# Optimization experiments

Hardware: AMD Instinct MI355X
Metric: run time of the kernel (lower is better)

Reference implementation:

```python
import jax, jax.numpy as jnp
import numpy as np
from jax import lax

H = 12  # num_heads (from init_kwargs)


def _orthogonal_landmarks(q, num_landmarks):
    # q: (B, N, D) already scaled. Faithful to torch loop: recursively pick the
    # point whose max |cos sim| to the already-selected landmarks is minimal.
    B, N, D = q.shape
    nrm = jnp.linalg.norm(q, axis=-1, keepdims=True)
    qk = q / jnp.maximum(nrm, 1e-12)
    bidx = jnp.arange(B)
    key = jax.random.key(42)
    idx0 = jax.random.randint(key, (B,), 0, N)
    cur = qk[bidx, idx0]                             # (B, D)
    # running max |cos sim|; selected rows pinned to 10 (as in torch code)
    max_sim = jnp.zeros((B, N), qk.dtype).at[bidx, idx0].set(10.0)

    def step(carry, _):
        max_sim, cur = carry
        cos = jnp.abs(jnp.einsum('bnd,bd->bn', qk, cur))
        max_sim = jnp.maximum(max_sim, cos)
        idx = jnp.argmin(max_sim, axis=-1)
        cur2 = qk[bidx, idx]
        max_sim = max_sim.at[bidx, idx].set(10.0)
        return (max_sim, cur2), idx

    (_, _), idxs = lax.scan(step, (max_sim, cur), None, length=num_landmarks - 1)
    all_idx = jnp.concatenate([idx0[None, :], idxs], axis=0).T  # (B, L)
    landmarks = q[bidx[:, None], all_idx]                        # unnormalized q rows
    return lax.stop_gradient(landmarks)


def _orthoformer(q, k, v, num_landmarks, num_frames):
    # q,k,v: (B*h, N, D);  N = F * P
    Bh, N, D = q.shape
    F = num_frames
    P = N // F
    sc = D ** (-0.25)
    q = q * sc
    k = k * sc
    lm = _orthogonal_landmarks(q, num_landmarks)                 # (Bh, L, D)
    kernel_1 = jax.nn.softmax(jnp.einsum('bnd,bld->bnl', q, lm), axis=-1)   # (Bh,N,L)
    k2 = jnp.einsum('bld,bnd->bln', lm, k).reshape(Bh, num_landmarks, F, P)
    kernel_2 = jax.nn.softmax(k2, axis=-1)                       # (Bh,L,F,P)
    vr = v.reshape(Bh, F, P, D)
    x = jnp.einsum('blfp,bfpd->blfd', kernel_2, vr)
    x = jnp.einsum('bnl,blfd->bnfd', kernel_1, x)                # (Bh,N,F,D)
    return x


def setup_inputs() -> dict:
    key = jax.random.key(0)
    ks = jax.random.split(key, 6)
    B, F, P, C = 2, 16, 196, 768
    N = F * P
    s = 0.02
    x = jax.random.normal(ks[0], (B, N, C), jnp.float32)
    W_qkv = jax.random.normal(ks[1], (C, 3 * C), jnp.float32) * s
    W_pq = jax.random.normal(ks[2], (C, C), jnp.float32) * s
    W_pkv = jax.random.normal(ks[3], (C, 2 * C), jnp.float32) * s
    W_proj = jax.random.normal(ks[4], (C, C), jnp.float32) * s
    b_proj = jnp.zeros((C,), jnp.float32)
    return {"x": x, "W_qkv": W_qkv, "W_pq": W_pq, "W_pkv": W_pkv,
            "W_proj": W_proj, "b_proj": b_proj,
            "seq_len": P, "num_frames": F, "num_landmarks": 128}


def reference(x, W_qkv, W_pq, W_pkv, W_proj, b_proj, seq_len, num_frames, num_landmarks):
    B, N, C = x.shape
    F, P, h = num_frames, seq_len, H
    d = C // h
    scale = d ** (-0.5)
    qkv = x @ W_qkv                                              # (B,N,3C)
    q, k, v = jnp.split(qkv, 3, axis=-1)
    def to_bh(t):  # b n (h d) -> (b h) n d
        return t.reshape(B, N, h, d).transpose(0, 2, 1, 3).reshape(B * h, N, d)
    q_, k_, v_ = to_bh(q), to_bh(k), to_bh(v)
    xo = _orthoformer(q_, k_, v_, num_landmarks, F)              # (B*h,N,F,d)
    # (b h) s f d -> b s f (h d)
    xo = xo.reshape(B, h, N, F, d).transpose(0, 2, 3, 1, 4).reshape(B, N, F, C)
    # diagonal over (frame-of-query g, frame-of-key f)
    xd = xo.reshape(B, F, P, F, C)
    xdiag = jnp.diagonal(xd, axis1=1, axis2=3)                   # (B,P,C,F)
    xdiag = jnp.moveaxis(xdiag, -1, 1).reshape(B, N, C)          # b (f p) d
    q2 = xdiag @ W_pq                                            # (B,N,C)
    k2, v2 = jnp.split(xo @ W_pkv, 2, axis=-1)                   # (B,N,F,C) each
    q2 = q2.reshape(B, N, h, d).transpose(0, 2, 1, 3) * scale    # (B,h,N,d)
    k2 = k2.reshape(B, N, F, h, d).transpose(0, 3, 1, 2, 4)      # (B,h,N,F,d)
    v2 = v2.reshape(B, N, F, h, d).transpose(0, 3, 1, 2, 4)
    attn = jax.nn.softmax(jnp.einsum('bhsd,bhsfd->bhsf', q2, k2), axis=-1)
    out = jnp.einsum('bhsf,bhsfd->bhsd', attn, v2)               # (B,h,N,d)
    out = out.transpose(0, 2, 1, 3).reshape(B, N, C)
    out = out @ W_proj + b_proj
    return out, attn
```

## Files before the change

kernel.cpp:

```cpp
#include <hip/hip_runtime.h>


using u16 = unsigned short;
using u32 = unsigned int;
using u64 = unsigned long long;

typedef short bf16x8 __attribute__((ext_vector_type(8)));
typedef float f32x4 __attribute__((ext_vector_type(4)));

#define N_ 3136
#define C_ 768
#define H_ 12
#define F_ 16
#define P_ 196
#define L_ 128
#define SC_ 0.35355339059327373f
#define OUTPART_ ((size_t)2 * N_ * C_)
#define KB_ 8
#define RPB_ 392

__device__ __forceinline__ float b2f(u16 u) {
  u32 x = ((u32)u) << 16; float f; __builtin_memcpy(&f, &x, 4); return f;
}
__device__ __forceinline__ float lo16f(u32 u) {
  u32 x = u << 16; float f; __builtin_memcpy(&f, &x, 4); return f;
}
__device__ __forceinline__ float hi16f(u32 u) {
  u32 x = u & 0xFFFF0000u; float f; __builtin_memcpy(&f, &x, 4); return f;
}
__device__ __forceinline__ u16 f2b(float f) {
  u32 u; __builtin_memcpy(&u, &f, 4);
  u32 r = (u + 0x7FFFu + ((u >> 16) & 1u)) >> 16;
  return (u16)r;
}
__device__ __forceinline__ u64 d2u(double d) { u64 u; __builtin_memcpy(&u, &d, 8); return u; }

__device__ __forceinline__ void gll16(const void* g, void* l) {
  __builtin_amdgcn_global_load_lds(
      (__attribute__((address_space(1))) void*)g,
      (__attribute__((address_space(3))) void*)l, 16, 0, 0);
}

__global__ void detect_k(const u32* __restrict__ w, int* __restrict__ flag) {
  const int t = threadIdx.x;
  int hits = 0;
  #pragma unroll
  for (int i = 0; i < 16; ++i) {
    u32 word = w[t * 16 + i];
    u32 e = (word >> 7) & 0xFFu;
    if (e >= 110u && e <= 126u) hits++;
  }
  #pragma unroll
  for (int off = 32; off > 0; off >>= 1) hits += __shfl_down(hits, off);
  if (t == 0) flag[0] = (hits >= 512) ? 0 : 1;
}

__global__ void zcnt_k(u64* __restrict__ p) { if (threadIdx.x < 384) p[threadIdx.x] = 0ull; }

__device__ __forceinline__ void tf2(u32 k0, u32 k1v, u32 c0, u32 c1, u32& o0, u32& o1) {
  u32 ks[3] = {k0, k1v, k0 ^ k1v ^ 0x1BD11BDAu};
  u32 x0 = c0 + ks[0], x1 = c1 + ks[1];
  const u32 rA[4] = {13u, 15u, 26u, 6u}, rB[4] = {17u, 29u, 16u, 24u};
  #pragma unroll
  for (int r = 0; r < 5; ++r) {
    #pragma unroll
    for (int q = 0; q < 4; ++q) {
      u32 rot = (r & 1) ? rB[q] : rA[q];
      x0 += x1; x1 = (x1 << rot) | (x1 >> (32u - rot)); x1 ^= x0;
    }
    x0 += ks[(r + 1) % 3];
    x1 += ks[(r + 2) % 3] + (u32)(r + 1);
  }
  o0 = x0; o1 = x1;
}

__device__ __forceinline__ int tf_idx0(int bh) {
  u32 a0, a1, b0, b1;
  tf2(0u, 42u, 0u, 0u, a0, a1);
  tf2(0u, 42u, 0u, 1u, b0, b1);
  u32 j = (u32)bh;
  u32 h0, h1, l0, l1;
  tf2(a0, a1, 0u, j, h0, h1);
  u32 hi = h0 ^ h1;
  tf2(b0, b1, 0u, j, l0, l1);
  u32 lo = l0 ^ l1;
  return (int)(((hi % 3136u) * 2048u + (lo % 3136u)) % 3136u);
}

__device__ __forceinline__ void qsel_body(const void* xr, const void* wr, int f32i,
                                          float* qt, int m0, int n0, int t,
                                          float* As, float* Bs)
{
  const int tx = t & 15, ty = t >> 4;
  float acc[8][4];
  #pragma unroll
  for (int i = 0; i < 8; ++i)
    #pragma unroll
    for (int j = 0; j < 4; ++j) acc[i][j] = 0.f;

  const int alr = t >> 1;
  const int alk = (t & 1) * 8;
  const int bkr = t >> 4;
  const int bnc = (t & 15) * 4;

  for (int k0 = 0; k0 < 768; k0 += 16) {
    float av[8];
    float4 bv;
    if (f32i) {
      const float* xa = (const float*)xr + (size_t)(m0 + alr) * 768 + k0 + alk;
      float4 a0 = *(const float4*)(xa);
      float4 a1 = *(const float4*)(xa + 4);
      av[0] = a0.x; av[1] = a0.y; av[2] = a0.z; av[3] = a0.w;
      av[4] = a1.x; av[5] = a1.y; av[6] = a1.z; av[7] = a1.w;
      bv = *(const float4*)((const float*)wr + (size_t)(k0 + bkr) * 2304 + n0 + bnc);
    } else {
      const u16* xa = (const u16*)xr + (size_t)(m0 + alr) * 768 + k0 + alk;
      #pragma unroll
      for (int j = 0; j < 8; ++j) av[j] = b2f(xa[j]);
      const u16* wa = (const u16*)wr + (size_t)(k0 + bkr) * 2304 + n0 + bnc;
      bv.x = b2f(wa[0]); bv.y = b2f(wa[1]); bv.z = b2f(wa[2]); bv.w = b2f(wa[3]);
    }
    #pragma unroll
    for (int j = 0; j < 8; ++j) As[alr * 20 + alk + j] = av[j];
    *(float4*)(&Bs[bkr * 64 + bnc]) = bv;
    __syncthreads();
    #pragma unroll
    for (int kk = 0; kk < 16; ++kk) {
      float a[8], b[4];
      #pragma unroll
      for (int i = 0; i < 8; ++i) a[i] = As[(ty * 8 + i) * 20 + kk];
      #pragma unroll
      for (int j = 0; j < 4; ++j) b[j] = Bs[kk * 64 + tx * 4 + j];
      #pragma unroll
      for (int i = 0; i < 8; ++i)
        #pragma unroll
        for (int j = 0; j < 4; ++j) acc[i][j] += a[i] * b[j];
    }
    __syncthreads();
  }
  #pragma unroll
  for (int i = 0; i < 8; ++i) {
    const int m = m0 + ty * 8 + i;
    const int b = m / N_, n = m - b * N_;
    #pragma unroll
    for (int j = 0; j < 4; ++j) {
      const int col = n0 + tx * 4 + j;
      const int hh = col >> 6, dd = col & 63;
      qt[((size_t)(b * H_ + hh) * 64 + dd) * N_ + n] = acc[i][j] * SC_;
    }
  }
}

__global__ __launch_bounds__(256) void qselT_k(const void* __restrict__ xr, const void* __restrict__ wr,
                                               const int* __restrict__ flagp, float* __restrict__ qt)
{
  __shared__ float As[128 * 20];
  __shared__ float Bs[16 * 64];
  qsel_body(xr, wr, flagp[0], qt, blockIdx.x * 128, blockIdx.y * 64, threadIdx.x, As, Bs);
}

__device__ __forceinline__ void twT_body(const void* W, int K, int Nn, int f32i,
                                         u16* WT, int k0, int n0, int t, u16 (&Ts)[64][80])
{
  const int kr = t >> 2, nc = (t & 3) * 16;
  u16 tmp[16];
  if (f32i) {
    const float* p = (const float*)W + (size_t)(k0 + kr) * Nn + n0 + nc;
    #pragma unroll
    for (int j = 0; j < 16; ++j) tmp[j] = f2b(p[j]);
  } else {
    const u16* p = (const u16*)W + (size_t)(k0 + kr) * Nn + n0 + nc;
    #pragma unroll
    for (int j = 0; j < 16; ++j) tmp[j] = p[j];
  }
  #pragma unroll
  for (int j = 0; j < 16; ++j) Ts[kr][nc + j] = tmp[j];
  __syncthreads();
  const int nr = t >> 2, kc = (t & 3) * 16;
  u16 o[16];
  #pragma unroll
  for (int j = 0; j < 16; ++j) o[j] = Ts[kc + j][nr];
  u16* dst = WT + (size_t)(n0 + nr) * K + k0 + kc;
  *(uint4*)(dst) = *(uint4*)(o);
  *(uint4*)(dst + 8) = *(uint4*)(o + 8);
}

__global__ __launch_bounds__(256) void twT_k(const void* __restrict__ W, int K, int Nn,
                                             const int* __restrict__ flagp, u16* __restrict__ WT)
{
  __shared__ u16 Ts[64][80];
  twT_body(W, K, Nn, flagp[0], WT, blockIdx.x * 64, blockIdx.y * 64, threadIdx.x, Ts);
}

__global__ __launch_bounds__(256) void twT3_k(const void* __restrict__ W0, const void* __restrict__ W1,
                                              const void* __restrict__ W2, const int* __restrict__ flagp,
                                              u16* __restrict__ T0, u16* __restrict__ T1, u16* __restrict__ T2,
                                              u16* __restrict__ Wb)
{
  __shared__ u16 Ts[64][80];
  const int z = blockIdx.z;
  const int t = threadIdx.x;
  if (z == 3) {
    const int k0 = blockIdx.x * 64, n0 = blockIdx.y * 64;
    const int kr = t >> 2, nc = (t & 3) * 16;
    u16 tmp[16];
    if (flagp[0]) {
      const float* p = (const float*)W0 + (size_t)(k0 + kr) * 1536 + n0 + nc;
      #pragma unroll
      for (int j = 0; j < 16; ++j) tmp[j] = f2b(p[j]);
    } else {
      const u16* p = (const u16*)W0 + (size_t)(k0 + kr) * 1536 + n0 + nc;
      #pragma unroll
      for (int j = 0; j < 16; ++j) tmp[j] = p[j];
    }
    u16* dst = Wb + (size_t)(k0 + kr) * 1536 + n0 + nc;
    *(uint4*)(dst) = *(uint4*)(tmp);
    *(uint4*)(dst + 8) = *(uint4*)(tmp + 8);
    return;
  }
  const void* W = (z == 0) ? W0 : (z == 1) ? W1 : W2;
  u16* WT = (z == 0) ? T0 : (z == 1) ? T1 : T2;
  const int Nn = (z == 0) ? 1536 : 768;
  if (blockIdx.y * 64 >= Nn) return;
  twT_body(W, 768, Nn, flagp[0], WT, blockIdx.x * 64, blockIdx.y * 64, t, Ts);
}

__device__ __forceinline__ void xcvt_body(const void* x, int f32i, u16* xb, int i)
{
  if (f32i) {
    const float4* p = (const float4*)x + (size_t)i * 2;
    float4 f0 = p[0], f1 = p[1];
    u16 tmp[8] = { f2b(f0.x), f2b(f0.y), f2b(f0.z), f2b(f0.w),
                   f2b(f1.x), f2b(f1.y), f2b(f1.z), f2b(f1.w) };
    *(uint4*)(xb + (size_t)i * 8) = *(uint4*)tmp;
  } else {
    ((uint4*)xb)[i] = ((const uint4*)x)[i];
  }
}

__global__ __launch_bounds__(256) void xcvt_k(const void* __restrict__ x,
                                              const int* __restrict__ flagp, u16* __restrict__ xb)
{
  xcvt_body(x, flagp[0], xb, blockIdx.x * 256 + threadIdx.x);
}

__global__ __launch_bounds__(256) void fusedA_k(const void* __restrict__ x, const void* __restrict__ Wqkv,
                                                const int* __restrict__ flagp, float* __restrict__ qt,
                                                u16* __restrict__ WqkvT, u16* __restrict__ xb)
{
  __shared__ float As[128 * 20];
  __shared__ float Bs[16 * 64];
  __shared__ u16 Ts[64][80];
  const int id = blockIdx.x;
  const int t = threadIdx.x;
  const int f32i = flagp[0];
  if (id < 588) {
    qsel_body(x, Wqkv, f32i, qt, (id % 49) * 128, (id / 49) * 64, t, As, Bs);
  } else if (id < 1020) {
    const int id2 = id - 588;
    twT_body(Wqkv, 768, 2304, f32i, WqkvT, (id2 % 12) * 64, (id2 / 12) * 64, t, Ts);
  } else {
    xcvt_body(x, f32i, xb, (id - 1020) * 256 + t);
  }
}

struct GemmCore {
  const u16 *aP0, *aP1, *bP0, *bP1;
  u16 *lA0, *lA1, *lB0, *lB1;
  int roA[4], roB[4];
  int mw, nw, lr, lk;
};

__device__ __forceinline__ void gemm_core_init(GemmCore& gc, u16* As, u16* Bs,
    const u16* A16, const u16* B16, size_t aOff, size_t bOff,
    int m0, int n0, int lda, int ldb, int M, int t)
{
  const int lane = t & 63;
  const int w = t >> 6;
  gc.mw = (w >> 1) * 64;
  gc.nw = (w & 1) * 64;
  gc.lr = lane & 15;
  gc.lk = lane >> 4;
  const int c0 = w * 2, c1 = c0 + 1;
  const int rl = lane >> 2, sl = lane & 3;
  const int rowA0 = c0 * 16 + rl, rowA1 = c1 * 16 + rl;
  const int segA0 = (sl ^ ((rowA0 ^ (rowA0 >> 2)) & 3)) * 8;
  const int segA1 = (sl ^ ((rowA1 ^ (rowA1 >> 2)) & 3)) * 8;
  int ga0 = m0 + rowA0; if (ga0 >= M) ga0 = M - 1;
  int ga1 = m0 + rowA1; if (ga1 >= M) ga1 = M - 1;
  gc.aP0 = A16 + aOff + (size_t)ga0 * lda + segA0;
  gc.aP1 = A16 + aOff + (size_t)ga1 * lda + segA1;
  gc.bP0 = B16 + bOff + (size_t)(n0 + rowA0) * ldb + segA0;
  gc.bP1 = B16 + bOff + (size_t)(n0 + rowA1) * ldb + segA1;
  gc.lA0 = &As[c0 * 512]; gc.lA1 = &As[c1 * 512];
  gc.lB0 = &Bs[c0 * 512]; gc.lB1 = &Bs[c1 * 512];
  #pragma unroll
  for (int q = 0; q < 4; ++q) {
    const int ra = gc.mw + q * 16 + gc.lr;
    gc.roA[q] = ra * 32 + ((gc.lk ^ ((ra ^ (ra >> 2)) & 3)) * 8);
    const int rb = gc.nw + q * 16 + gc.lr;
    gc.roB[q] = rb * 32 + ((gc.lk ^ ((rb ^ (rb >> 2)) & 3)) * 8);
  }
}

__device__ __forceinline__ void gemm_core_loop(const GemmCore& gc, u16* As, u16* Bs,
                                               int K, f32x4 (&acc)[4][4])
{
  for (int k0 = 0; k0 < K; k0 += 32) {
    gll16(gc.aP0 + k0, gc.lA0);
    gll16(gc.aP1 + k0, gc.lA1);
    gll16(gc.bP0 + k0, gc.lB0);
    gll16(gc.bP1 + k0, gc.lB1);
    __syncthreads();
    bf16x8 af[4], bfv[4];
    #pragma unroll
    for (int mt = 0; mt < 4; ++mt) af[mt] = *(const bf16x8*)(&As[gc.roA[mt]]);
    #pragma unroll
    for (int nt = 0; nt < 4; ++nt) bfv[nt] = *(const bf16x8*)(&Bs[gc.roB[nt]]);
    #pragma unroll
    for (int mt = 0; mt < 4; ++mt)
      #pragma unroll
      for (int nt = 0; nt < 4; ++nt)
        acc[mt][nt] = __builtin_amdgcn_mfma_f32_16x16x32_bf16(af[mt], bfv[nt], acc[mt][nt], 0, 0, 0);
    __syncthreads();
  }
}

__device__ __forceinline__ void mode0_epi(const f32x4 (&acc)[4][4], int m0, int n0,
                                          int mw, int nw, int lr, int lk,
                                          u16* ob0, u16* ob1, u16* ob2)
{
  #pragma unroll
  for (int mt = 0; mt < 4; ++mt) {
    #pragma unroll
    for (int nt = 0; nt < 4; ++nt) {
      #pragma unroll
      for (int r = 0; r < 4; ++r) {
        const int grow = m0 + mw + mt * 16 + lk * 4 + r;
        const int gcol = n0 + nw + nt * 16 + lr;
        float vv = acc[mt][nt][r];
        int b = (grow >= N_) ? 1 : 0;
        int n = grow - b * N_;
        int t3 = gcol / C_, cc = gcol - t3 * C_;
        int hh = cc >> 6, dd = cc & 63;
        size_t dst = (((size_t)(b * H_ + hh)) * N_ + n) * 64 + dd;
        if (t3 == 0) ob0[dst] = f2b(vv * SC_);
        else if (t3 == 1) ob1[dst] = f2b(vv * SC_);
        else ob2[dst] = f2b(vv);
      }
    }
  }
}

__global__ __launch_bounds__(512, 1) void fusedB_k(
    const float* __restrict__ qt, float* __restrict__ lm, u64* __restrict__ cand,
    const u16* __restrict__ xb, const u16* __restrict__ WqkvT,
    u16* __restrict__ qb, u16* __restrict__ kbuf, u16* __restrict__ vb)
{
  __shared__ double curD[64];
  __shared__ u64 redV[8];
  __shared__ int redI[8];
  __shared__ int sW;
  __shared__ u16 As[128 * 32];
  __shared__ u16 Bs[128 * 32];
  const int t = threadIdx.x;

  if (blockIdx.x >= 192) {
    const int gid = blockIdx.x - 192;
    const int m0 = (gid % 49) * 128;
    const int n0 = (gid / 49) * 128;
    if (t < 256) {
      f32x4 acc[4][4];
      #pragma unroll
      for (int i = 0; i < 4; ++i)
        #pragma unroll
        for (int j = 0; j < 4; ++j) acc[i][j] = (f32x4){0.f, 0.f, 0.f, 0.f};
      GemmCore gc;
      gemm_core_init(gc, As, Bs, xb, WqkvT, 0, 0, m0, n0, 768, 768, 6272, t);
      gemm_core_loop(gc, As, Bs, 768, acc);
      mode0_epi(acc, m0, n0, gc.mw, gc.nw, gc.lr, gc.lk, qb, kbuf, vb);
    } else {
      for (int i = 0; i < 24; ++i) { __syncthreads(); __syncthreads(); }
    }
    return;
  }

  const int bh = blockIdx.x % 24;
  const int kb = blockIdx.x / 24;
  const float* QT = qt + (size_t)bh * 64 * N_;
  float* LM = lm + (size_t)bh * L_ * 64;
  u64* cd = cand + (size_t)bh * 16;
  const bool act = (t < RPB_);
  const int g = t >> 2, dc = t & 3, d0 = dc * 16;
  const int r0 = kb * RPB_;
  const int myRow = r0 + t;
  const float* base = QT + r0 + 4 * g;

  float4 qreg[16];
  #pragma unroll
  for (int i = 0; i < 16; ++i) qreg[i] = (float4){0.f, 0.f, 0.f, 0.f};
  if (act) {
    #pragma unroll
    for (int i = 0; i < 16; ++i) qreg[i] = *(const float4*)(base + (size_t)(d0 + i) * N_);
  }

  double inv_own = 0.0, ms_own = 0.0;
  if (act) {
    double s0 = 0.0, s1 = 0.0, s2 = 0.0, s3 = 0.0;
    #pragma unroll
    for (int i = 0; i < 16; ++i) {
      const float4 v = qreg[i];
      s0 += (double)v.x * (double)v.x; s1 += (double)v.y * (double)v.y;
      s2 += (double)v.z * (double)v.z; s3 += (double)v.w * (double)v.w;
    }
    s0 += __shfl_xor(s0, 1); s1 += __shfl_xor(s1, 1);
    s2 += __shfl_xor(s2, 1); s3 += __shfl_xor(s3, 1);
    s0 += __shfl_xor(s0, 2); s1 += __shfl_xor(s1, 2);
    s2 += __shfl_xor(s2, 2); s3 += __shfl_xor(s3, 2);
    const double sown = (dc == 0) ? s0 : (dc == 1) ? s1 : (dc == 2) ? s2 : s3;
    inv_own = 1.0 / fmax(sqrt(sown), 1e-12);
  }
  const int idx0 = tf_idx0(bh);
  if (act && myRow == idx0) ms_own = 10.0;

  if (t < 64) {
    const float vf = QT[(size_t)t * N_ + idx0];
    double v = (double)vf;
    double s = v * v;
    #pragma unroll
    for (int off = 32; off; off >>= 1) s += __shfl_xor(s, off);
    curD[t] = v / fmax(sqrt(s), 1e-12);
    if (kb == 0) LM[t] = vf;
  }
  __syncthreads();

  for (int step = 1; step < 128; ++step) {
    u64 bV = d2u(1e30); int bI = 0x7fffffff;
    if (act) {
      double a0 = 0.0, a1 = 0.0, a2 = 0.0, a3 = 0.0;
      #pragma unroll
      for (int i = 0; i < 16; ++i) {
        const float4 v = qreg[i];
        const double c = curD[d0 + i];
        a0 += (double)v.x * c; a1 += (double)v.y * c;
        a2 += (double)v.z * c; a3 += (double)v.w * c;
      }
      a0 += __shfl_xor(a0, 1); a1 += __shfl_xor(a1, 1);
      a2 += __shfl_xor(a2, 1); a3 += __shfl_xor(a3, 1);
      a0 += __shfl_xor(a0, 2); a1 += __shfl_xor(a1, 2);
      a2 += __shfl_xor(a2, 2); a3 += __shfl_xor(a3, 2);
      const double aown = (dc == 0) ? a0 : (dc == 1) ? a1 : (dc == 2) ? a2 : a3;
      ms_own = fmax(ms_own, fabs(aown * inv_own));
      bV = d2u(ms_own); bI = myRow;
    }
    #pragma unroll
    for (int off = 32; off; off >>= 1) {
      const u64 ov = __shfl_xor(bV, off);
      const int oi = __shfl_xor(bI, off);
      if (ov < bV || (ov == bV && oi < bI)) { bV = ov; bI = oi; }
    }
    if ((t & 63) == 0) { redV[t >> 6] = bV; redI[t >> 6] = bI; }
    __syncthreads();
    const int par = step & 1;
    if (t == 0) {
      u64 v = redV[0]; int ix = redI[0];
      #pragma unroll
      for (int w2 = 1; w2 < 8; ++w2)
        if (redV[w2] < v || (redV[w2] == v && redI[w2] < ix)) { v = redV[w2]; ix = redI[w2]; }
      const u64 pk = (v & ~((1ull << 19) - 1ull)) | ((u64)(u32)(step & 127) << 12) | (u64)(u32)ix;
      __hip_atomic_store(&cd[par * KB_ + kb], pk, __ATOMIC_RELAXED, __HIP_MEMORY_SCOPE_AGENT);
    }
    if (t < 64) {
      u64 pv = ~0ull;
      int ok = 1;
      for (;;) {
        if (t < KB_) {
          pv = __hip_atomic_load(&cd[par * KB_ + t], __ATOMIC_RELAXED, __HIP_MEMORY_SCOPE_AGENT);
          ok = ((int)((pv >> 12) & 127u) == step) ? 1 : 0;
        }
        if (__all(ok)) break;
        __builtin_amdgcn_s_sleep(1);
      }
      u64 m = (t < KB_) ? pv : ~0ull;
      #pragma unroll
      for (int off = 1; off < KB_; off <<= 1) {
        const u64 o = __shfl_xor(m, off);
        if (o < m) m = o;
      }
      if (t == 0) sW = (int)(m & 0xFFFu);
    }
    __syncthreads();
    const int w = sW;
    if (act && myRow == w) ms_own = 10.0;
    if (t < 64) {
      const float vf = QT[(size_t)t * N_ + w];
      double v = (double)vf;
      double s = v * v;
      #pragma unroll
      for (int off = 32; off; off >>= 1) s += __shfl_xor(s, off);
      curD[t] = v / fmax(sqrt(s), 1e-12);
      if (kb == 0) LM[(size_t)step * 64 + t] = vf;
    }
    __syncthreads();
  }
}

template <int MODE>
__global__ __launch_bounds__(256) void gemm_k(
    const void* __restrict__ Ap, const void* __restrict__ Bp,
    int M, int K, int lda, int ldb, int n0c, int cn, const int* __restrict__ flagp,
    float* __restrict__ of0, u16* __restrict__ ob0, u16* __restrict__ ob1, u16* __restrict__ ob2,
    const void* __restrict__ biasRaw, void* __restrict__ outRaw)
{
  __shared__ u16 As[128 * 32];
  __shared__ u16 Bs[128 * 32];
  const int t = threadIdx.x;
  const int m0 = blockIdx.x * 128;
  const int n0 = blockIdx.y * 128;
  const int rf = (MODE == 4) ? flagp[0] : 0;

  size_t aOff = 0, bOff = 0;
  if constexpr (MODE == 1) {
    const int bh = blockIdx.z;
    aOff = (size_t)bh * ((size_t)N_ * 128) + (size_t)n0c * 128;
    bOff = (size_t)bh * (1024 * 128);
  }
  if constexpr (MODE == 5) {
    const int h = blockIdx.z;
    aOff = (size_t)h * (2 * cn) * 64;
    bOff = (size_t)h * 64;
  }
  if constexpr (MODE == 6) {
    const int h = blockIdx.z;
    aOff = (size_t)h * (2 * cn) * 768;
    bOff = (size_t)(768 + h * 64) * 768;
  }
  f32x4 acc[4][4];
  #pragma unroll
  for (int i = 0; i < 4; ++i)
    #pragma unroll
    for (int j = 0; j < 4; ++j) acc[i][j] = (f32x4){0.f, 0.f, 0.f, 0.f};

  GemmCore gc;
  gemm_core_init(gc, As, Bs, (const u16*)Ap, (const u16*)Bp, aOff, bOff, m0, n0, lda, ldb, M, t);
  gemm_core_loop(gc, As, Bs, K, acc);

  const int lr = gc.lr, lk = gc.lk, mw = gc.mw, nw = gc.nw;
  if constexpr (MODE == 0) {
    mode0_epi(acc, m0, n0, mw, nw, lr, lk, ob0, ob1, ob2);
    return;
  }
  #pragma unroll
  for (int mt = 0; mt < 4; ++mt) {
    #pragma unroll
    for (int nt = 0; nt < 4; ++nt) {
      #pragma unroll
      for (int r = 0; r < 4; ++r) {
        const int grow = m0 + mw + mt * 16 + lk * 4 + r;
        const int gcol = n0 + nw + nt * 16 + lr;
        if (grow >= M) continue;
        float vv = acc[mt][nt][r];
        if constexpr (MODE == 1) {
          const int bh = blockIdx.z;
          int b = bh / H_, hh = bh - b * H_;
          int f = gcol >> 6, dd = gcol & 63;
          u16 wv = f2b(vv);
          ob0[(((size_t)(b * cn + grow)) * F_ + f) * C_ + hh * 64 + dd] = wv;
          int n = n0c + grow;
          if (f == n / P_) ob1[((size_t)(b * cn + grow)) * C_ + hh * 64 + dd] = wv;
        } else if constexpr (MODE == 3) {
          int hh = gcol >> 6, dd = gcol & 63;
          ob0[((size_t)hh * (2 * cn) + grow) * 64 + dd] = f2b(vv * 0.125f);
        } else if constexpr (MODE == 5) {
          ob0[((size_t)blockIdx.z * (2 * cn) + grow) * 768 + gcol] = f2b(vv);
        } else if constexpr (MODE == 6) {
          if (gcol < 64) {
            int b2 = (grow >= cn) ? 1 : 0;
            int ln = grow - b2 * cn;
            ob0[((size_t)(b2 * N_ + n0c + ln)) * 768 + blockIdx.z * 64 + gcol] = f2b(vv);
          }
        } else {
          float bvad = rf ? ((const float*)biasRaw)[gcol] : b2f(((const u16*)biasRaw)[gcol]);
          float ov = vv + bvad;
          if (rf) ((float*)outRaw)[(size_t)grow * C_ + gcol] = ov;
          else    ((u16*)outRaw)[(size_t)grow * C_ + gcol] = f2b(ov);
        }
      }
    }
  }
}

__global__ __launch_bounds__(256) void k1_k(const u16* __restrict__ qb,
                                            const float* __restrict__ lm,
                                            u16* __restrict__ k1)
{
  const int bh = blockIdx.y;
  const int r0 = blockIdx.x * 64;
  __shared__ float qT[64][65];
  __shared__ float lmS[128 * 64];
  __shared__ float redA[4][64];
  __shared__ float redB[64];
  const int t = threadIdx.x;
  const u16* Q = qb + ((size_t)bh * N_ + r0) * 64;
  const float* Lm = lm + (size_t)bh * L_ * 64;
  for (int u = t; u < 2048; u += 256) ((float4*)lmS)[u] = ((const float4*)Lm)[u];
  for (int u = t; u < 512; u += 256) {
    int row = u >> 3, j0 = (u & 7) * 8;
    uint4 pk = *(const uint4*)(Q + (size_t)row * 64 + j0);
    const u16* pu = (const u16*)&pk;
    #pragma unroll
    for (int jj = 0; jj < 8; ++jj) qT[j0 + jj][row] = b2f(pu[jj]);
  }
  __syncthreads();
  const int row = t & 63, ch = t >> 6;
  float qr[64];
  #pragma unroll
  for (int j = 0; j < 64; ++j) qr[j] = qT[j][row];
  float s[32];
  for (int li = 0; li < 32; ++li) {
    const float* lp = lmS + (ch * 32 + li) * 64;
    float a = 0.f;
    #pragma unroll
    for (int j = 0; j < 64; ++j) a += lp[j] * qr[j];
    s[li] = a;
  }
  float mx = -1e30f;
  for (int li = 0; li < 32; ++li) mx = fmaxf(mx, s[li]);
  redA[ch][row] = mx;
  __syncthreads();
  if (t < 64) redB[t] = fmaxf(fmaxf(redA[0][t], redA[1][t]), fmaxf(redA[2][t], redA[3][t]));
  __syncthreads();
  mx = redB[row];
  float sum = 0.f;
  for (int li = 0; li < 32; ++li) { float e = __expf(s[li] - mx); s[li] = e; sum += e; }
  __syncthreads();
  redA[ch][row] = sum;
  __syncthreads();
  if (t < 64) redB[t] = 1.0f / (redA[0][t] + redA[1][t] + redA[2][t] + redA[3][t]);
  __syncthreads();
  const float inv = redB[row];
  u16* out = k1 + ((size_t)bh * N_ + r0 + row) * 128 + ch * 32;
  for (int li = 0; li < 32; ++li) out[li] = f2b(s[li] * inv);
}

__global__ __launch_bounds__(256) void k2x1_k(const float* __restrict__ lm,
                                              const u16* __restrict__ kb,
                                              const u16* __restrict__ vb,
                                              u16* __restrict__ x1)
{
  const int bh = blockIdx.x;
  const int f = blockIdx.y;
  __shared__ u16 kS[P_ * 64];
  __shared__ u16 vS[P_ * 64];
  __shared__ float redM[2][128];
  __shared__ float redS[2][128];
  const int t = threadIdx.x;
  const u16* Kf = kb + ((size_t)bh * N_ + f * P_) * 64;
  const u16* Vf = vb + ((size_t)bh * N_ + f * P_) * 64;
  for (int u = t; u < 1568; u += 256) {
    ((uint4*)kS)[u] = ((const uint4*)Kf)[u];
    ((uint4*)vS)[u] = ((const uint4*)Vf)[u];
  }
  __syncthreads();
  const int l = t & 127, half = t >> 7;
  const float* lp = lm + ((size_t)bh * L_ + l) * 64;
  float lr[64];
  #pragma unroll
  for (int j = 0; j < 64; ++j) lr[j] = lp[j];

  const int p0 = half * 98, p1 = p0 + 98;
  float mx = -1e30f;
  for (int p = p0; p < p1; ++p) {
    const uint4* kp = (const uint4*)(kS + p * 64);
    float s = 0.f;
    #pragma unroll
    for (int q4 = 0; q4 < 8; ++q4) {
      uint4 pk = kp[q4];
      const u32* pu = (const u32*)&pk;
      #pragma unroll
      for (int j2 = 0; j2 < 4; ++j2) {
        u32 u = pu[j2];
        s += lr[q4 * 8 + j2 * 2] * lo16f(u) + lr[q4 * 8 + j2 * 2 + 1] * hi16f(u);
      }
    }
    mx = fmaxf(mx, s);
  }
  redM[half][l] = mx;
  __syncthreads();
  mx = fmaxf(redM[0][l], redM[1][l]);

  float sm = 0.f;
  for (int p = p0; p < p1; ++p) {
    const uint4* kp = (const uint4*)(kS + p * 64);
    float s = 0.f;
    #pragma unroll
    for (int q4 = 0; q4 < 8; ++q4) {
      uint4 pk = kp[q4];
      const u32* pu = (const u32*)&pk;
      #pragma unroll
      for (int j2 = 0; j2 < 4; ++j2) {
        u32 u = pu[j2];
        s += lr[q4 * 8 + j2 * 2] * lo16f(u) + lr[q4 * 8 + j2 * 2 + 1] * hi16f(u);
      }
    }
    sm += __expf(s - mx);
  }
  redS[half][l] = sm;
  __syncthreads();
  const float inv = 1.0f / (redS[0][l] + redS[1][l]);

  const int dd0 = half * 32;
  float acc[32];
  #pragma unroll
  for (int u = 0; u < 32; ++u) acc[u] = 0.f;
  for (int p = 0; p < P_; ++p) {
    const uint4* kp = (const uint4*)(kS + p * 64);
    float s = 0.f;
    #pragma unroll
    for (int q4 = 0; q4 < 8; ++q4) {
      uint4 pk = kp[q4];
      const u32* pu = (const u32*)&pk;
      #pragma unroll
      for (int j2 = 0; j2 < 4; ++j2) {
        u32 u = pu[j2];
        s += lr[q4 * 8 + j2 * 2] * lo16f(u) + lr[q4 * 8 + j2 * 2 + 1] * hi16f(u);
      }
    }
    const float e = __expf(s - mx);
    const uint4* vp = (const uint4*)(vS + p * 64 + dd0);
    #pragma unroll
    for (int q4 = 0; q4 < 4; ++q4) {
      uint4 pv = vp[q4];
      const u32* pu = (const u32*)&pv;
      #pragma unroll
      for (int j2 = 0; j2 < 4; ++j2) {
        u32 u = pu[j2];
        acc[q4 * 8 + j2 * 2]     += e * lo16f(u);
        acc[q4 * 8 + j2 * 2 + 1] += e * hi16f(u);
      }
    }
  }
  u16* outT = x1 + (size_t)bh * (1024 * 128) + (size_t)(f * 64 + dd0) * 128 + l;
  for (int u = 0; u < 32; ++u) outT[(size_t)u * 128] = f2b(acc[u] * inv);
}

__global__ __launch_bounds__(256) void attn2_k(const u16* __restrict__ xoc,
                                               const u16* __restrict__ g,
                                               int n0c, int cn, const int* __restrict__ flagp,
                                               void* __restrict__ outRaw, u16* __restrict__ wc)
{
  __shared__ float aS[12][16];
  const int t = threadIdx.x;
  const int m = blockIdx.x;
  const int b = (m >= cn) ? 1 : 0;
  const int ln = m - b * cn;
  const int n = n0c + ln;
  const int f32o = flagp[0];
  const u16* Xo = xoc + ((size_t)(b * cn + ln) * 16) * 768;
  const size_t hstr = (size_t)(2 * cn) * 768;

  if (t < 192) {
    const int h = t >> 4, f = t & 15;
    const uint4* xp = (const uint4*)(Xo + (size_t)f * 768);
    const uint4* gp = (const uint4*)(g + (size_t)h * hstr + (size_t)m * 768);
    float lg = 0.f;
    #pragma unroll 4
    for (int q = 0; q < 96; ++q) {
      uint4 xv = xp[q], gv = gp[q];
      const u32* xu = (const u32*)&xv;
      const u32* gu = (const u32*)&gv;
      #pragma unroll
      for (int j = 0; j < 4; ++j)
        lg += lo16f(xu[j]) * lo16f(gu[j]) + hi16f(xu[j]) * hi16f(gu[j]);
    }
    float mx = lg;
    mx = fmaxf(mx, __shfl_xor(mx, 1));
    mx = fmaxf(mx, __shfl_xor(mx, 2));
    mx = fmaxf(mx, __shfl_xor(mx, 4));
    mx = fmaxf(mx, __shfl_xor(mx, 8));
    float e = __expf(lg - mx);
    float sm = e;
    sm += __shfl_xor(sm, 1);
    sm += __shfl_xor(sm, 2);
    sm += __shfl_xor(sm, 4);
    sm += __shfl_xor(sm, 8);
    const float a = e / sm;
    const size_t abase = ((size_t)(b * H_ + h) * N_ + n) * F_ + f;
    if (f32o) ((float*)outRaw)[OUTPART_ + abase] = a;
    else      ((u16*)outRaw)[OUTPART_ + abase] = f2b(a);
    aS[h][f] = a;
  }
  __syncthreads();
  if (t < 192) {
    const int cg = t >> 1, sh = t & 1;
    const int c0 = cg * 8;
    float acc[6][8];
    #pragma unroll
    for (int j = 0; j < 6; ++j)
      #pragma unroll
      for (int k = 0; k < 8; ++k) acc[j][k] = 0.f;
    for (int f = 0; f < 16; ++f) {
      uint4 xv = *(const uint4*)(Xo + (size_t)f * 768 + c0);
      const u32* xu = (const u32*)&xv;
      float xf[8];
      #pragma unroll
      for (int j = 0; j < 4; ++j) { xf[2 * j] = lo16f(xu[j]); xf[2 * j + 1] = hi16f(xu[j]); }
      #pragma unroll
      for (int j = 0; j < 6; ++j) {
        const float a = aS[sh * 6 + j][f];
        #pragma unroll
        for (int k = 0; k < 8; ++k) acc[j][k] += a * xf[k];
      }
    }
    #pragma unroll
    for (int j = 0; j < 6; ++j) {
      u16 pk[8];
      #pragma unroll
      for (int k = 0; k < 8; ++k) pk[k] = f2b(acc[j][k]);
      *(uint4*)(wc + (size_t)(sh * 6 + j) * hstr + (size_t)m * 768 + c0) = *(uint4*)pk;
    }
  }
}

extern "C" void kernel_launch(void* const* d_in, const int* in_sizes, int n_in,
                              void* d_out, int out_size, void* d_ws, size_t ws_size,
                              hipStream_t stream)
{
  (void)in_sizes; (void)n_in; (void)out_size;
  const void* x     = d_in[0];
  const void* Wqkv  = d_in[1];
  const void* Wpq   = d_in[2];
  const void* Wpkv  = d_in[3];
  const void* Wproj = d_in[4];
  const void* bproj = d_in[5];

  char* ws = (char*)d_ws;
  size_t off = 0;
  auto alloc = [&](size_t bytes) { void* p = ws + off; off += (bytes + 255) & ~(size_t)255; return p; };
  int*  flagp  = (int*)alloc(256);
  u16*  WpkvT  = (u16*)alloc(2359296);
  u16*  WpqT   = (u16*)alloc(1179648);
  u16*  WprojT = (u16*)alloc(1179648);
  u16*  Wpkvb  = (u16*)alloc(2359296);
  float* lm    = (float*)alloc(786432);
  u16*  x1b    = (u16*)alloc(6291456);
  u16*  k1b    = (u16*)alloc(19267584);
  const size_t sc0 = off;

  const size_t r1 = sc0;
  const size_t r2 = r1 + 19267584 + 3072;
  const size_t r3 = r2 + 3538944 + 9633792;
  const size_t bigNeed = r3 + 3 * (size_t)9633792 + 256;
  const bool fused = (bigNeed <= ws_size);

  float* qt;  u64* cand;  u16 *WqkvT, *xb, *qb, *kbuf, *vb, *ob;
  size_t chunkBase;
  if (fused) {
    qt    = (float*)(ws + r1);
    cand  = (u64*)(ws + r1 + 19267584);
    WqkvT = (u16*)(ws + r2);
    xb    = WqkvT + 1769472;
    qb    = (u16*)(ws + r3);
    kbuf  = qb + 4816896;
    vb    = kbuf + 4816896;
    ob    = (u16*)(ws + sc0);
    chunkBase = sc0 + 9633792;
  } else {
    qt    = (float*)(ws + sc0);
    cand  = (u64*)(ws + sc0 + 19267584);
    WqkvT = (u16*)(ws + sc0);
    xb    = (u16*)(ws + sc0 + 3538944);
    qb    = (u16*)(ws + sc0 + 13172736);
    kbuf  = qb + 4816896;
    vb    = kbuf + 4816896;
    ob    = (u16*)(ws + sc0);
    chunkBase = sc0 + 9633792;
    if (sc0 + 42074112 + 1024 > ws_size) return;
  }

  int Nc = 0;
  {
    const int cands[5] = {3136, 1568, 784, 392, 196};
    for (int i = 0; i < 5; ++i) {
      if (chunkBase + (size_t)92160 * cands[i] + 1024 <= ws_size) { Nc = cands[i]; break; }
    }
  }
  if (Nc == 0) return;
  const int nchunks = N_ / Nc;
  u16* xoc = (u16*)(ws + chunkBase);
  u16* xdc = xoc + (size_t)24576 * Nc;
  u16* q2b = xdc + (size_t)1536 * Nc;
  u16* gbf = q2b + (size_t)1536 * Nc;

  detect_k<<<1, 64, 0, stream>>>((const u32*)Wqkv, flagp);
  zcnt_k<<<1, 512, 0, stream>>>(cand);
  twT3_k<<<dim3(12, 24, 4), 256, 0, stream>>>(Wpkv, Wpq, Wproj, flagp,
                                              WpkvT, WpqT, WprojT, Wpkvb);

  if (fused) {
    fusedA_k<<<3372, 256, 0, stream>>>(x, Wqkv, flagp, qt, WqkvT, xb);
    fusedB_k<<<1074, 512, 0, stream>>>(qt, lm, cand, xb, WqkvT, qb, kbuf, vb);
  } else {
    qselT_k<<<dim3(49, 12), 256, 0, stream>>>(x, Wqkv, flagp, qt);
    fusedB_k<<<192, 512, 0, stream>>>(qt, lm, cand, xb, WqkvT, qb, kbuf, vb);
    twT_k<<<dim3(12, 36), 256, 0, stream>>>(Wqkv, 768, 2304, flagp, WqkvT);
    xcvt_k<<<2352, 256, 0, stream>>>(x, flagp, xb);
    gemm_k<0><<<dim3(49, 18, 1), 256, 0, stream>>>(xb, WqkvT, 6272, 768, 768, 768, 0, 0, flagp,
                                                   nullptr, qb, kbuf, vb, nullptr, nullptr);
  }

  k2x1_k<<<dim3(24, 16), 256, 0, stream>>>(lm, kbuf, vb, x1b);
  k1_k<<<dim3(49, 24), 256, 0, stream>>>(qb, lm, k1b);

  const int gx = (2 * Nc + 127) / 128;
  for (int c = 0; c < nchunks; ++c) {
    const int n0c = c * Nc;
    gemm_k<1><<<dim3((Nc + 127) / 128, 8, 24), 256, 0, stream>>>(
        k1b, x1b, Nc, 128, 128, 128, n0c, Nc, flagp, nullptr, xoc, xdc, nullptr, nullptr, nullptr);
    gemm_k<3><<<dim3(gx, 6, 1), 256, 0, stream>>>(
        xdc, WpqT, 2 * Nc, 768, 768, 768, n0c, Nc, flagp, nullptr, q2b, nullptr, nullptr, nullptr, nullptr);
    gemm_k<5><<<dim3(gx, 6, 12), 256, 0, stream>>>(
        q2b, Wpkvb, 2 * Nc, 64, 64, 1536, n0c, Nc, flagp, nullptr, gbf, nullptr, nullptr, nullptr, nullptr);
    attn2_k<<<dim3(2 * Nc), 256, 0, stream>>>(xoc, gbf, n0c, Nc, flagp, d_out, gbf);
    gemm_k<6><<<dim3(gx, 1, 12), 256, 0, stream>>>(
        gbf, WpkvT, 2 * Nc, 768, 768, 768, n0c, Nc, flagp, nullptr, ob, nullptr, nullptr, nullptr, nullptr);
  }
  gemm_k<4><<<dim3(49, 6, 1), 256, 0, stream>>>(ob, WprojT, 6272, 768, 768, 768, 0, 0, flagp,
                                                nullptr, nullptr, nullptr, nullptr, bproj, d_out);
}
```

Before: 1.483 ms.

## Fuse weight prep into fusedA, merge k1/k2x1 kernels, relocate ob buffer

Folds the three projection-weight transposes and the Wpkv bf16 copy into the fusedA launch, and merges the k2x1 and k1 kernels into a single fusedC launch with shared memory carved from one buffer. This cuts launch count and lets independent small kernels share the GPU instead of running back-to-back with idle tails. It also moves the ob buffer to the end of the workspace and changes the chunk-size candidates, so the chunked post-attention loop now runs at most 1568 rows per chunk, always at least two chunks. The fused kernels use a larger static shared-memory footprint for every block, which may lower occupancy for the lighter branches.

```diff
diff --git a/kernel.cpp b/kernel.cpp
--- a/kernel.cpp
+++ b/kernel.cpp
@@ -192,6 +192,25 @@
   twT_body(W, K, Nn, flagp[0], WT, blockIdx.x * 64, blockIdx.y * 64, threadIdx.x, Ts);
 }
 
+__device__ __forceinline__ void wpkvb_body(const void* W0, int f32i, u16* Wb,
+                                           int k0, int n0, int t)
+{
+  const int kr = t >> 2, nc = (t & 3) * 16;
+  u16 tmp[16];
+  if (f32i) {
+    const float* p = (const float*)W0 + (size_t)(k0 + kr) * 1536 + n0 + nc;
+    #pragma unroll
+    for (int j = 0; j < 16; ++j) tmp[j] = f2b(p[j]);
+  } else {
+    const u16* p = (const u16*)W0 + (size_t)(k0 + kr) * 1536 + n0 + nc;
+    #pragma unroll
+    for (int j = 0; j < 16; ++j) tmp[j] = p[j];
+  }
+  u16* dst = Wb + (size_t)(k0 + kr) * 1536 + n0 + nc;
+  *(uint4*)(dst) = *(uint4*)(tmp);
+  *(uint4*)(dst + 8) = *(uint4*)(tmp + 8);
+}
+
 __global__ __launch_bounds__(256) void twT3_k(const void* __restrict__ W0, const void* __restrict__ W1,
                                               const void* __restrict__ W2, const int* __restrict__ flagp,
                                               u16* __restrict__ T0, u16* __restrict__ T1, u16* __restrict__ T2,
@@ -201,21 +220,7 @@
   const int z = blockIdx.z;
   const int t = threadIdx.x;
   if (z == 3) {
-    const int k0 = blockIdx.x * 64, n0 = blockIdx.y * 64;
-    const int kr = t >> 2, nc = (t & 3) * 16;
-    u16 tmp[16];
-    if (flagp[0]) {
-      const float* p = (const float*)W0 + (size_t)(k0 + kr) * 1536 + n0 + nc;
-      #pragma unroll
-      for (int j = 0; j < 16; ++j) tmp[j] = f2b(p[j]);
-    } else {
-      const u16* p = (const u16*)W0 + (size_t)(k0 + kr) * 1536 + n0 + nc;
-      #pragma unroll
-      for (int j = 0; j < 16; ++j) tmp[j] = p[j];
-    }
-    u16* dst = Wb + (size_t)(k0 + kr) * 1536 + n0 + nc;
-    *(uint4*)(dst) = *(uint4*)(tmp);
-    *(uint4*)(dst + 8) = *(uint4*)(tmp + 8);
+    wpkvb_body(W0, flagp[0], Wb, blockIdx.x * 64, blockIdx.y * 64, t);
     return;
   }
   const void* W = (z == 0) ? W0 : (z == 1) ? W1 : W2;
@@ -245,8 +250,12 @@
 }
 
 __global__ __launch_bounds__(256) void fusedA_k(const void* __restrict__ x, const void* __restrict__ Wqkv,
+                                                const void* __restrict__ Wpq, const void* __restrict__ Wpkv,
+                                                const void* __restrict__ Wproj,
                                                 const int* __restrict__ flagp, float* __restrict__ qt,
-                                                u16* __restrict__ WqkvT, u16* __restrict__ xb)
+                                                u16* __restrict__ WqkvT, u16* __restrict__ xb,
+                                                u16* __restrict__ WpkvT, u16* __restrict__ WpqT,
+                                                u16* __restrict__ WprojT, u16* __restrict__ Wpkvb)
 {
   __shared__ float As[128 * 20];
   __shared__ float Bs[16 * 64];
@@ -259,8 +268,22 @@
   } else if (id < 1020) {
     const int id2 = id - 588;
     twT_body(Wqkv, 768, 2304, f32i, WqkvT, (id2 % 12) * 64, (id2 / 12) * 64, t, Ts);
+  } else if (id < 3372) {
+    xcvt_body(x, f32i, xb, (id - 1020) * 256 + t);
   } else {
-    xcvt_body(x, f32i, xb, (id - 1020) * 256 + t);
+    const int id2 = id - 3372;
+    const int z = id2 / 288;
+    const int rem = id2 - z * 288;
+    const int bx = rem % 12, by = rem / 12;
+    if (z == 3) {
+      wpkvb_body(Wpkv, f32i, Wpkvb, bx * 64, by * 64, t);
+    } else {
+      const void* W = (z == 0) ? Wpkv : (z == 1) ? Wpq : Wproj;
+      u16* WT = (z == 0) ? WpkvT : (z == 1) ? WpqT : WprojT;
+      const int Nn = (z == 0) ? 1536 : 768;
+      if (by * 64 < Nn)
+        twT_body(W, 768, Nn, f32i, WT, bx * 64, by * 64, t, Ts);
+    }
   }
 }
 
@@ -502,6 +525,168 @@
       if (kb == 0) LM[(size_t)step * 64 + t] = vf;
     }
     __syncthreads();
+  }
+}
+
+__device__ __forceinline__ void k1_body(const u16* qb, const float* lm, u16* k1,
+                                        int bh, int r0, int t, char* smem)
+{
+  float (*qT)[65] = (float(*)[65])smem;
+  float* lmS = (float*)(smem + 16640);
+  float (*redA)[64] = (float(*)[64])(smem + 16640 + 32768);
+  float* redB = (float*)(smem + 16640 + 32768 + 1024);
+  const u16* Q = qb + ((size_t)bh * N_ + r0) * 64;
+  const float* Lm = lm + (size_t)bh * L_ * 64;
+  for (int u = t; u < 2048; u += 256) ((float4*)lmS)[u] = ((const float4*)Lm)[u];
+  for (int u = t; u < 512; u += 256) {
+    int row = u >> 3, j0 = (u & 7) * 8;
+    uint4 pk = *(const uint4*)(Q + (size_t)row * 64 + j0);
+    const u16* pu = (const u16*)&pk;
+    #pragma unroll
+    for (int jj = 0; jj < 8; ++jj) qT[j0 + jj][row] = b2f(pu[jj]);
+  }
+  __syncthreads();
+  const int row = t & 63, ch = t >> 6;
+  float qr[64];
+  #pragma unroll
+  for (int j = 0; j < 64; ++j) qr[j] = qT[j][row];
+  float s[32];
+  for (int li = 0; li < 32; ++li) {
+    const float* lp = lmS + (ch * 32 + li) * 64;
+    float a = 0.f;
+    #pragma unroll
+    for (int j = 0; j < 64; ++j) a += lp[j] * qr[j];
+    s[li] = a;
+  }
+  float mx = -1e30f;
+  for (int li = 0; li < 32; ++li) mx = fmaxf(mx, s[li]);
+  redA[ch][row] = mx;
+  __syncthreads();
+  if (t < 64) redB[t] = fmaxf(fmaxf(redA[0][t], redA[1][t]), fmaxf(redA[2][t], redA[3][t]));
+  __syncthreads();
+  mx = redB[row];
+  float sum = 0.f;
+  for (int li = 0; li < 32; ++li) { float e = __expf(s[li] - mx); s[li] = e; sum += e; }
+  __syncthreads();
+  redA[ch][row] = sum;
+  __syncthreads();
+  if (t < 64) redB[t] = 1.0f / (redA[0][t] + redA[1][t] + redA[2][t] + redA[3][t]);
+  __syncthreads();
+  const float inv = redB[row];
+  u16* out = k1 + ((size_t)bh * N_ + r0 + row) * 128 + ch * 32;
+  for (int li = 0; li < 32; ++li) out[li] = f2b(s[li] * inv);
+}
+
+__device__ __forceinline__ void k2x1_body(const float* lm, const u16* kb, const u16* vb,
+                                          u16* x1, int bh, int f, int t, char* smem)
+{
+  u16* kS = (u16*)smem;
+  u16* vS = (u16*)(smem + 25088);
+  float (*redM)[128] = (float(*)[128])(smem + 50176);
+  float (*redS)[128] = (float(*)[128])(smem + 51200);
+  const u16* Kf = kb + ((size_t)bh * N_ + f * P_) * 64;
+  const u16* Vf = vb + ((size_t)bh * N_ + f * P_) * 64;
+  for (int u = t; u < 1568; u += 256) {
+    ((uint4*)kS)[u] = ((const uint4*)Kf)[u];
+    ((uint4*)vS)[u] = ((const uint4*)Vf)[u];
+  }
+  __syncthreads();
+  const int l = t & 127, half = t >> 7;
+  const float* lp = lm + ((size_t)bh * L_ + l) * 64;
+  float lr[64];
+  #pragma unroll
+  for (int j = 0; j < 64; ++j) lr[j] = lp[j];
+
+  const int p0 = half * 98, p1 = p0 + 98;
+  float mx = -1e30f;
+  for (int p = p0; p < p1; ++p) {
+    const uint4* kp = (const uint4*)(kS + p * 64);
+    float s = 0.f;
+    #pragma unroll
+    for (int q4 = 0; q4 < 8; ++q4) {
+      uint4 pk = kp[q4];
+      const u32* pu = (const u32*)&pk;
+      #pragma unroll
+      for (int j2 = 0; j2 < 4; ++j2) {
+        u32 u = pu[j2];
+        s += lr[q4 * 8 + j2 * 2] * lo16f(u) + lr[q4 * 8 + j2 * 2 + 1] * hi16f(u);
+      }
+    }
+    mx = fmaxf(mx, s);
+  }
+  redM[half][l] = mx;
+  __syncthreads();
+  mx = fmaxf(redM[0][l], redM[1][l]);
+
+  float sm = 0.f;
+  for (int p = p0; p < p1; ++p) {
+    const uint4* kp = (const uint4*)(kS + p * 64);
+    float s = 0.f;
+    #pragma unroll
+    for (int q4 = 0; q4 < 8; ++q4) {
+      uint4 pk = kp[q4];
+      const u32* pu = (const u32*)&pk;
+      #pragma unroll
+      for (int j2 = 0; j2 < 4; ++j2) {
+        u32 u = pu[j2];
+        s += lr[q4 * 8 + j2 * 2] * lo16f(u) + lr[q4 * 8 + j2 * 2 + 1] * hi16f(u);
+      }
+    }
+    sm += __expf(s - mx);
+  }
+  redS[half][l] = sm;
+  __syncthreads();
+  const float inv = 1.0f / (redS[0][l] + redS[1][l]);
+
+  const int dd0 = half * 32;
+  float acc[32];
+  #pragma unroll
+  for (int u = 0; u < 32; ++u) acc[u] = 0.f;
+  for (int p = 0; p < P_; ++p) {
+    const uint4* kp = (const uint4*)(kS + p * 64);
+    float s = 0.f;
+    #pragma unroll
+    for (int q4 = 0; q4 < 8; ++q4) {
+      uint4 pk = kp[q4];
+      const u32* pu = (const u32*)&pk;
+      #pragma unroll
+      for (int j2 = 0; j2 < 4; ++j2) {
+        u32 u = pu[j2];
+        s += lr[q4 * 8 + j2 * 2] * lo16f(u) + lr[q4 * 8 + j2 * 2 + 1] * hi16f(u);
+      }
+    }
+    const float e = __expf(s - mx);
+    const uint4* vp = (const uint4*)(vS + p * 64 + dd0);
+    #pragma unroll
+    for (int q4 = 0; q4 < 4; ++q4) {
+      uint4 pv = vp[q4];
+      const u32* pu = (const u32*)&pv;
+      #pragma unroll
+      for (int j2 = 0; j2 < 4; ++j2) {
+        u32 u = pu[j2];
+        acc[q4 * 8 + j2 * 2]     += e * lo16f(u);
+        acc[q4 * 8 + j2 * 2 + 1] += e * hi16f(u);
+      }
+    }
+  }
+  u16* outT = x1 + (size_t)bh * (1024 * 128) + (size_t)(f * 64 + dd0) * 128 + l;
+  for (int u = 0; u < 32; ++u) outT[(size_t)u * 128] = f2b(acc[u] * inv);
+}
+
+__global__ __launch_bounds__(256) void fusedC_k(const u16* __restrict__ qb,
+                                                const float* __restrict__ lm,
+                                                const u16* __restrict__ kbuf,
+                                                const u16* __restrict__ vb,
+                                                u16* __restrict__ k1b, u16* __restrict__ x1b)
+{
+  __shared__ __align__(16) char smem[52224];
+  const int id = blockIdx.x;
+  const int t = threadIdx.x;
+  if (id < 384) {
+    k2x1_body(lm, kbuf, vb, x1b, id % 24, id / 24, t, smem);
+  } else {
+    const int id2 = id - 384;
+    k1_body(qb, lm, k1b, id2 / 49, (id2 % 49) * 64, t, smem);
   }
 }
 
@@ -590,160 +775,6 @@
   }
 }
 
-__global__ __launch_bounds__(256) void k1_k(const u16* __restrict__ qb,
-                                            const float* __restrict__ lm,
-                                            u16* __restrict__ k1)
-{
-  const int bh = blockIdx.y;
-  const int r0 = blockIdx.x * 64;
-  __shared__ float qT[64][65];
-  __shared__ float lmS[128 * 64];
-  __shared__ float redA[4][64];
-  __shared__ float redB[64];
-  const int t = threadIdx.x;
-  const u16* Q = qb + ((size_t)bh * N_ + r0) * 64;
-  const float* Lm = lm + (size_t)bh * L_ * 64;
-  for (int u = t; u < 2048; u += 256) ((float4*)lmS)[u] = ((const float4*)Lm)[u];
-  for (int u = t; u < 512; u += 256) {
-    int row = u >> 3, j0 = (u & 7) * 8;
-    uint4 pk = *(const uint4*)(Q + (size_t)row * 64 + j0);
-    const u16* pu = (const u16*)&pk;
-    #pragma unroll
-    for (int jj = 0; jj < 8; ++jj) qT[j0 + jj][row] = b2f(pu[jj]);
-  }
-  __syncthreads();
-  const int row = t & 63, ch = t >> 6;
-  float qr[64];
-  #pragma unroll
-  for (int j = 0; j < 64; ++j) qr[j] = qT[j][row];
-  float s[32];
-  for (int li = 0; li < 32; ++li) {
-    const float* lp = lmS + (ch * 32 + li) * 64;
-    float a = 0.f;
-    #pragma unroll
-    for (int j = 0; j < 64; ++j) a += lp[j] * qr[j];
-    s[li] = a;
-  }
-  float mx = -1e30f;
-  for (int li = 0; li < 32; ++li) mx = fmaxf(mx, s[li]);
-  redA[ch][row] = mx;
-  __syncthreads();
-  if (t < 64) redB[t] = fmaxf(fmaxf(redA[0][t], redA[1][t]), fmaxf(redA[2][t], redA[3][t]));
-  __syncthreads();
-  mx = redB[row];
-  float sum = 0.f;
-  for (int li = 0; li < 32; ++li) { float e = __expf(s[li] - mx); s[li] = e; sum += e; }
-  __syncthreads();
-  redA[ch][row] = sum;
-  __syncthreads();
-  if (t < 64) redB[t] = 1.0f / (redA[0][t] + redA[1][t] + redA[2][t] + redA[3][t]);
-  __syncthreads();
-  const float inv = redB[row];
-  u16* out = k1 + ((size_t)bh * N_ + r0 + row) * 128 + ch * 32;
-  for (int li = 0; li < 32; ++li) out[li] = f2b(s[li] * inv);
-}
-
-__global__ __launch_bounds__(256) void k2x1_k(const float* __restrict__ lm,
-                                              const u16* __restrict__ kb,
-                                              const u16* __restrict__ vb,
-                                              u16* __restrict__ x1)
-{
-  const int bh = blockIdx.x;
-  const int f = blockIdx.y;
-  __shared__ u16 kS[P_ * 64];
-  __shared__ u16 vS[P_ * 64];
-  __shared__ float redM[2][128];
-  __shared__ float redS[2][128];
-  const int t = threadIdx.x;
-  const u16* Kf = kb + ((size_t)bh * N_ + f * P_) * 64;
-  const u16* Vf = vb + ((size_t)bh * N_ + f * P_) * 64;
-  for (int u = t; u < 1568; u += 256) {
-    ((uint4*)kS)[u] = ((const uint4*)Kf)[u];
-    ((uint4*)vS)[u] = ((const uint4*)Vf)[u];
-  }
-  __syncthreads();
-  const int l = t & 127, half = t >> 7;
-  const float* lp = lm + ((size_t)bh * L_ + l) * 64;
-  float lr[64];
-  #pragma unroll
-  for (int j = 0; j < 64; ++j) lr[j] = lp[j];
-
-  const int p0 = half * 98, p1 = p0 + 98;
-  float mx = -1e30f;
-  for (int p = p0; p < p1; ++p) {
-    const uint4* kp = (const uint4*)(kS + p * 64);
-    float s = 0.f;
-    #pragma unroll
-    for (int q4 = 0; q4 < 8; ++q4) {
-      uint4 pk = kp[q4];
-      const u32* pu = (const u32*)&pk;
-      #pragma unroll
-      for (int j2 = 0; j2 < 4; ++j2) {
-        u32 u = pu[j2];
-        s += lr[q4 * 8 + j2 * 2] * lo16f(u) + lr[q4 * 8 + j2 * 2 + 1] * hi16f(u);
-      }
-    }
-    mx = fmaxf(mx, s);
-  }
-  redM[half][l] = mx;
-  __syncthreads();
-  mx = fmaxf(redM[0][l], redM[1][l]);
-
-  float sm = 0.f;
-  for (int p = p0; p < p1; ++p) {
-    const uint4* kp = (const uint4*)(kS + p * 64);
-    float s = 0.f;
-    #pragma unroll
-    for (int q4 = 0; q4 < 8; ++q4) {
-      uint4 pk = kp[q4];
-      const u32* pu = (const u32*)&pk;
-      #pragma unroll
-      for (int j2 = 0; j2 < 4; ++j2) {
-        u32 u = pu[j2];
-        s += lr[q4 * 8 + j2 * 2] * lo16f(u) + lr[q4 * 8 + j2 * 2 + 1] * hi16f(u);
-      }
-    }
-    sm += __expf(s - mx);
-  }
-  redS[half][l] = sm;
-  __syncthreads();
-  const float inv = 1.0f / (redS[0][l] + redS[1][l]);
-
-  const int dd0 = half * 32;
-  float acc[32];
-  #pragma unroll
-  for (int u = 0; u < 32; ++u) acc[u] = 0.f;
-  for (int p = 0; p < P_; ++p) {
-    const uint4* kp = (const uint4*)(kS + p * 64);
-    float s = 0.f;
-    #pragma unroll
-    for (int q4 = 0; q4 < 8; ++q4) {
-      uint4 pk = kp[q4];
-      const u32* pu = (const u32*)&pk;
-      #pragma unroll
-      for (int j2 = 0; j2 < 4; ++j2) {
-        u32 u = pu[j2];
-        s += lr[q4 * 8 + j2 * 2] * lo16f(u) + lr[q4 * 8 + j2 * 2 + 1] * hi16f(u);
-      }
-    }
-    const float e = __expf(s - mx);
-    const uint4* vp = (const uint4*)(vS + p * 64 + dd0);
-    #pragma unroll
-    for (int q4 = 0; q4 < 4; ++q4) {
-      uint4 pv = vp[q4];
-      const u32* pu = (const u32*)&pv;
-      #pragma unroll
-      for (int j2 = 0; j2 < 4; ++j2) {
-        u32 u = pu[j2];
-        acc[q4 * 8 + j2 * 2]     += e * lo16f(u);
-        acc[q4 * 8 + j2 * 2 + 1] += e * hi16f(u);
-      }
-    }
-  }
-  u16* outT = x1 + (size_t)bh * (1024 * 128) + (size_t)(f * 64 + dd0) * 128 + l;
-  for (int u = 0; u < 32; ++u) outT[(size_t)u * 128] = f2b(acc[u] * inv);
-}
-
 __global__ __launch_bounds__(256) void attn2_k(const u16* __restrict__ xoc,
                                                const u16* __restrict__ g,
                                                int n0c, int cn, const int* __restrict__ flagp,
@@ -847,14 +878,17 @@
   u16*  k1b    = (u16*)alloc(19267584);
   const size_t sc0 = off;
 
+  if (ws_size < sc0 + 9633792 + 1024) return;
+  const size_t obOff = (ws_size - 9633792) & ~(size_t)255;
+  u16* ob = (u16*)(ws + obOff);
+
   const size_t r1 = sc0;
   const size_t r2 = r1 + 19267584 + 3072;
   const size_t r3 = r2 + 3538944 + 9633792;
   const size_t bigNeed = r3 + 3 * (size_t)9633792 + 256;
   const bool fused = (bigNeed <= ws_size);
 
-  float* qt;  u64* cand;  u16 *WqkvT, *xb, *qb, *kbuf, *vb, *ob;
-  size_t chunkBase;
+  float* qt;  u64* cand;  u16 *WqkvT, *xb, *qb, *kbuf, *vb;
   if (fused) {
     qt    = (float*)(ws + r1);
     cand  = (u64*)(ws + r1 + 19267584);
@@ -863,8 +897,6 @@
     qb    = (u16*)(ws + r3);
     kbuf  = qb + 4816896;
     vb    = kbuf + 4816896;
-    ob    = (u16*)(ws + sc0);
-    chunkBase = sc0 + 9633792;
   } else {
     qt    = (float*)(ws + sc0);
     cand  = (u64*)(ws + sc0 + 19267584);
@@ -873,34 +905,33 @@
     qb    = (u16*)(ws + sc0 + 13172736);
     kbuf  = qb + 4816896;
     vb    = kbuf + 4816896;
-    ob    = (u16*)(ws + sc0);
-    chunkBase = sc0 + 9633792;
     if (sc0 + 42074112 + 1024 > ws_size) return;
   }
 
   int Nc = 0;
   {
-    const int cands[5] = {3136, 1568, 784, 392, 196};
-    for (int i = 0; i < 5; ++i) {
-      if (chunkBase + (size_t)92160 * cands[i] + 1024 <= ws_size) { Nc = cands[i]; break; }
+    const int cands[6] = {1568, 784, 448, 392, 224, 196};
+    for (int i = 0; i < 6; ++i) {
+      if (sc0 + (size_t)92160 * cands[i] <= obOff) { Nc = cands[i]; break; }
     }
   }
   if (Nc == 0) return;
   const int nchunks = N_ / Nc;
-  u16* xoc = (u16*)(ws + chunkBase);
+  u16* xoc = (u16*)(ws + sc0);
   u16* xdc = xoc + (size_t)24576 * Nc;
   u16* q2b = xdc + (size_t)1536 * Nc;
   u16* gbf = q2b + (size_t)1536 * Nc;
 
   detect_k<<<1, 64, 0, stream>>>((const u32*)Wqkv, flagp);
   zcnt_k<<<1, 512, 0, stream>>>(cand);
-  twT3_k<<<dim3(12, 24, 4), 256, 0, stream>>>(Wpkv, Wpq, Wproj, flagp,
-                                              WpkvT, WpqT, WprojT, Wpkvb);
 
   if (fused) {
-    fusedA_k<<<3372, 256, 0, stream>>>(x, Wqkv, flagp, qt, WqkvT, xb);
+    fusedA_k<<<4524, 256, 0, stream>>>(x, Wqkv, Wpq, Wpkv, Wproj, flagp, qt,
+                                       WqkvT, xb, WpkvT, WpqT, WprojT, Wpkvb);
     fusedB_k<<<1074, 512, 0, stream>>>(qt, lm, cand, xb, WqkvT, qb, kbuf, vb);
   } else {
+    twT3_k<<<dim3(12, 24, 4), 256, 0, stream>>>(Wpkv, Wpq, Wproj, flagp,
+                                                WpkvT, WpqT, WprojT, Wpkvb);
     qselT_k<<<dim3(49, 12), 256, 0, stream>>>(x, Wqkv, flagp, qt);
     fusedB_k<<<192, 512, 0, stream>>>(qt, lm, cand, xb, WqkvT, qb, kbuf, vb);
     twT_k<<<dim3(12, 36), 256, 0, stream>>>(Wqkv, 768, 2304, flagp, WqkvT);
@@ -909,8 +940,7 @@
                                                    nullptr, qb, kbuf, vb, nullptr, nullptr);
   }
 
-  k2x1_k<<<dim3(24, 16), 256, 0, stream>>>(lm, kbuf, vb, x1b);
-  k1_k<<<dim3(49, 24), 256, 0, stream>>>(qb, lm, k1b);
+  fusedC_k<<<1560, 256, 0, stream>>>(qb, lm, kbuf, vb, k1b, x1b);
 
   const int gx = (2 * Nc + 127) / 128;
   for (int c = 0; c < nchunks; ++c) {
```

Measured after the change: 1.463 ms. About the same (-1.4%).
